# Performance work log

Hardware: AMD Instinct MI355X
Metric: run time of the kernel (lower is better)

Reference implementation:

```python
import jax, jax.numpy as jnp
import numpy as np

N = 50000      # nodes
E = 800000     # edges (avg degree 16)
IN, HID, OUT = 128, 128, 64


def setup_inputs() -> dict:
    key = jax.random.key(0)
    ks = jax.random.split(key, 6)
    x = jax.random.normal(ks[0], (N, IN), dtype=jnp.float32)
    edge_index = jax.random.randint(ks[1], (2, E), 0, N, dtype=jnp.int32)
    # GCNConv params (glorot-ish scaling)
    W1 = jax.random.normal(ks[2], (IN, HID), dtype=jnp.float32) * (1.0 / np.sqrt(IN))
    b1 = jnp.zeros((HID,), dtype=jnp.float32)
    W2 = jax.random.normal(ks[3], (HID, OUT), dtype=jnp.float32) * (1.0 / np.sqrt(HID))
    b2 = jnp.zeros((OUT,), dtype=jnp.float32)
    return {"x": x, "edge_index": edge_index, "W1": W1, "b1": b1, "W2": W2, "b2": b2}


def _gcn_conv(h, edge_index, W, b):
    """PyG GCNConv: linear transform, then sym-normalized aggregation with self-loops."""
    h = h @ W  # [N, out]
    src, dst = edge_index[0], edge_index[1]
    # degree including the added self-loop
    deg = jax.ops.segment_sum(jnp.ones((E,), h.dtype), dst, num_segments=N) + 1.0
    dinv = jax.lax.rsqrt(deg)                       # deg^{-1/2}
    norm = dinv[src] * dinv[dst]                    # [E]
    agg = jax.ops.segment_sum(h[src] * norm[:, None], dst, num_segments=N)
    agg = agg + h * (dinv * dinv)[:, None]          # self-loop term: deg^{-1} * h_i
    return agg + b


def reference(x, edge_index, W1, b1, W2, b2):
    h = jax.nn.relu(_gcn_conv(x, edge_index, W1, b1))
    h = jax.nn.relu(_gcn_conv(h, edge_index, W2, b2))
    return h
```

## Files before the change

kernel.cpp:

```cpp
#include <hip/hip_runtime.h>

#define DIN 128
#define DHID 128
#define DOUT 64
#define CAPB 6144
#define CHUNK 4096
#define EPT (CHUNK / 256)

typedef short bf16x8 __attribute__((ext_vector_type(8)));
typedef float f32x4 __attribute__((ext_vector_type(4)));

static __device__ __forceinline__ unsigned short f2bf(float f) {
  union { float f; unsigned u; } v; v.f = f;
  unsigned r = v.u + 0x7fffu + ((v.u >> 16) & 1u);
  return (unsigned short)(r >> 16);
}
static __device__ __forceinline__ float bf_lo(unsigned v) {
  union { unsigned u; float f; } t; t.u = v << 16; return t.f;
}
static __device__ __forceinline__ float bf_hi(unsigned v) {
  union { unsigned u; float f; } t; t.u = v & 0xffff0000u; return t.f;
}
static __device__ __forceinline__ float bf1(unsigned short v) {
  union { unsigned u; float f; } t; t.u = ((unsigned)v) << 16; return t.f;
}

static __device__ __forceinline__ void wcast_body(
    const float* __restrict__ W, unsigned short* __restrict__ Wf,
    int NOUT, int tid) {
  int f = tid >> 6;
  int lane = tid & 63;
  int t = f & 3;
  int nt = f >> 2;
  int kbase = t * 32 + (lane >> 4) * 8;
  int n = nt * 16 + (lane & 15);
#pragma unroll
  for (int j = 0; j < 8; ++j)
    Wf[(size_t)tid * 8 + j] = f2bf(W[(size_t)(kbase + j) * NOUT + n]);
}

__global__ __launch_bounds__(256) void init_kernel(
    const float* __restrict__ W1, const float* __restrict__ W2,
    unsigned short* __restrict__ Wf1, unsigned short* __restrict__ Wf2,
    int* __restrict__ bincursor) {
  const int b = blockIdx.x;
  const int t = threadIdx.x;
  if (b == 0) {
    bincursor[t] = 0;
  } else if (b <= 8) {
    wcast_body(W1, Wf1, DHID, (b - 1) * 256 + t);
  } else {
    wcast_body(W2, Wf2, DOUT, (b - 9) * 256 + t);
  }
}

static __device__ void gemm1_tile(
    const float* __restrict__ A, const unsigned short* __restrict__ Wf,
    unsigned short* __restrict__ C, int M, int tile) {
  constexpr int NT = DHID / 16;
  const int lane = threadIdx.x & 63;
  const int wave = threadIdx.x >> 6;
  const int g = lane >> 4;
  const int m15 = lane & 15;

  bf16x8 bfrag[NT * 4];
#pragma unroll
  for (int f = 0; f < NT * 4; ++f)
    bfrag[f] = *(const bf16x8*)(Wf + ((size_t)(f * 64 + lane)) * 8);

  const int rowbase = tile * 64 + wave * 16;
  if (rowbase >= M) return;
  f32x4 acc[NT];
#pragma unroll
  for (int nt = 0; nt < NT; ++nt) acc[nt] = (f32x4){0.f, 0.f, 0.f, 0.f};
  const float* arow = A + (size_t)(rowbase + m15) * 128 + g * 8;
  bf16x8 af[4];
#pragma unroll
  for (int t = 0; t < 4; ++t) {
    float4 a0 = *(const float4*)(arow + t * 32);
    float4 a1 = *(const float4*)(arow + t * 32 + 4);
    bf16x8 f;
    f[0] = (short)f2bf(a0.x); f[1] = (short)f2bf(a0.y);
    f[2] = (short)f2bf(a0.z); f[3] = (short)f2bf(a0.w);
    f[4] = (short)f2bf(a1.x); f[5] = (short)f2bf(a1.y);
    f[6] = (short)f2bf(a1.z); f[7] = (short)f2bf(a1.w);
    af[t] = f;
  }
#pragma unroll
  for (int t = 0; t < 4; ++t)
#pragma unroll
    for (int nt = 0; nt < NT; ++nt)
      acc[nt] = __builtin_amdgcn_mfma_f32_16x16x32_bf16(
          af[t], bfrag[nt * 4 + t], acc[nt], 0, 0, 0);
#pragma unroll
  for (int nt = 0; nt < NT; ++nt)
#pragma unroll
    for (int r = 0; r < 4; ++r) {
      int row = rowbase + g * 4 + r;
      if (row < M)
        C[(size_t)row * DHID + nt * 16 + m15] = f2bf(acc[nt][r]);
    }
}

__global__ __launch_bounds__(256) void phaseA_kernel(
    const int* __restrict__ src, const int* __restrict__ dst,
    int* __restrict__ bincursor, unsigned* __restrict__ binbuf, int E,
    int nbinA, const float* __restrict__ x,
    const unsigned short* __restrict__ Wf1, unsigned short* __restrict__ h1,
    int M) {
  __shared__ int hist[256];
  __shared__ int cnt[256];
  __shared__ int offs[256];
  __shared__ int cur[256];
  __shared__ int gbase[256];
  __shared__ unsigned stage[CHUNK];

  if ((int)blockIdx.x >= nbinA) {
    gemm1_tile(x, Wf1, h1, M, (int)blockIdx.x - nbinA);
    return;
  }

  const int t = threadIdx.x;
  const int base = blockIdx.x * CHUNK;
  const int n = min(CHUNK, E - base);

  hist[t] = 0;
  __syncthreads();

  unsigned rec[EPT];
  int rng[EPT];
#pragma unroll
  for (int j = 0; j < EPT; ++j) {
    int e = base + j * 256 + t;
    rng[j] = -1;
    if (e < E) {
      int d = dst[e];
      int s = src[e];
      int r = d >> 8;
      rng[j] = r;
      rec[j] = (unsigned)s | ((unsigned)(d & 255) << 16) | ((unsigned)r << 24);
      atomicAdd(&hist[r], 1);
    }
  }
  __syncthreads();
  int myc = hist[t];
  cnt[t] = myc;
  __syncthreads();
#pragma unroll
  for (int o = 1; o < 256; o <<= 1) {
    int u = (t >= o) ? hist[t - o] : 0;
    __syncthreads();
    hist[t] += u;
    __syncthreads();
  }
  offs[t] = hist[t] - myc;
  cur[t] = hist[t] - myc;
  __syncthreads();
#pragma unroll
  for (int j = 0; j < EPT; ++j) {
    if (rng[j] >= 0) {
      int pos = atomicAdd(&cur[rng[j]], 1);
      stage[pos] = rec[j];
    }
  }
  __syncthreads();
  int c = cnt[t];
  gbase[t] = c ? atomicAdd(&bincursor[t], c) : 0;
  __syncthreads();
  for (int i = t; i < n; i += 256) {
    unsigned v = stage[i];
    int r = v >> 24;
    int local = i - offs[r];
    int gpos = gbase[r] + local;
    if (gpos < CAPB) binbuf[(size_t)r * CAPB + gpos] = v & 0x00ffffffu;
  }
}

__global__ __launch_bounds__(256) void scan_local_kernel(
    const unsigned* __restrict__ binbuf, const int* __restrict__ bincursor,
    int* __restrict__ rowptr, int* __restrict__ bsum,
    float* __restrict__ dinv, int n) {
  __shared__ int deg[256];
  __shared__ int lds[256];
  const int t = threadIdx.x;
  const int b = blockIdx.x;
  deg[t] = 0;
  __syncthreads();
  const int cnt = min(bincursor[b], CAPB);
  const unsigned* seg = binbuf + (size_t)b * CAPB;
  for (int i = t; i < cnt; i += 256) atomicAdd(&deg[(seg[i] >> 16) & 0xff], 1);
  __syncthreads();
  const int i = b * 256 + t;
  int v = (i < n) ? deg[t] : 0;
  if (i < n) dinv[i] = rsqrtf((float)v + 1.0f);
  lds[t] = v;
  __syncthreads();
#pragma unroll
  for (int o = 1; o < 256; o <<= 1) {
    int u = (t >= o) ? lds[t - o] : 0;
    __syncthreads();
    lds[t] += u;
    __syncthreads();
  }
  if (i < n) rowptr[i] = lds[t] - v;
  if (t == 255) bsum[b] = lds[255];
}

__global__ __launch_bounds__(256) void scan_add_kernel(
    int* __restrict__ rowptr, const int* __restrict__ bsum, int nr,
    int n, int E) {
  __shared__ int lds[256];
  const int t = threadIdx.x;
  int v = (t < nr) ? bsum[t] : 0;
  lds[t] = v;
  __syncthreads();
#pragma unroll
  for (int o = 1; o < 256; o <<= 1) {
    int u = (t >= o) ? lds[t - o] : 0;
    __syncthreads();
    lds[t] += u;
    __syncthreads();
  }
  const int off = (blockIdx.x == 0) ? 0 : lds[blockIdx.x - 1];
  const int i = blockIdx.x * 256 + t;
  if (i < n) rowptr[i] += off;
  if (i == n) rowptr[n] = E;
}

__global__ __launch_bounds__(256) void binB_kernel(
    const unsigned* __restrict__ binbuf, const int* __restrict__ bincursor,
    const int* __restrict__ rowptr, const float* __restrict__ dinv,
    unsigned* __restrict__ recs, int n) {
  __shared__ int curs[256];
  __shared__ unsigned stage[CAPB];
  const int t = threadIdx.x;
  const int r = blockIdx.x;
  const int n0 = r * 256;
  const int nn = min(256, n - n0);
  const int segbase = rowptr[n0];
  if (t < nn) curs[t] = rowptr[n0 + t] - segbase;
  __syncthreads();
  const int cnt = min(bincursor[r], CAPB);
  const unsigned* seg = binbuf + (size_t)r * CAPB;
  for (int i = t; i < cnt; i += 256) {
    unsigned v = seg[i];
    int s = v & 0xffffu;
    int dl = (v >> 16) & 0xff;
    float w = dinv[s] * dinv[n0 + dl];
    int pos = atomicAdd(&curs[dl], 1);
    stage[pos] = (unsigned)s | ((unsigned)f2bf(w) << 16);
  }
  __syncthreads();
  for (int i = t; i < cnt; i += 256) recs[segbase + i] = stage[i];
}

__global__ __launch_bounds__(256) void agg1_gemm2_kernel(
    const unsigned short* __restrict__ h, const unsigned* __restrict__ recs,
    const int* __restrict__ rowptr, const float* __restrict__ dinv,
    const float* __restrict__ b1, const unsigned short* __restrict__ Wf2,
    unsigned short* __restrict__ h2, int n) {
  __shared__ unsigned short tile[16][136];
  const int wave = threadIdx.x >> 6;
  const int lane = threadIdx.x & 63;
  const int nbase = blockIdx.x * 16;
  const unsigned col = lane * 2;
  const float2 bv = *(const float2*)(b1 + col);

  for (int q = 0; q < 4; ++q) {
    const int row = wave * 4 + q;
    const int nid = nbase + row;
    if (nid >= n) break;
    const float di = dinv[nid];
    int p = rowptr[nid];
    const int end = rowptr[nid + 1];
    float ax = 0.f, ay = 0.f;
    for (; p < end && (p & 3); ++p) {
      unsigned r = recs[p];
      float w = bf_hi(r);
      unsigned v = *(const unsigned*)(h + (size_t)(r & 0xffffu) * 128 + col);
      ax += bf_lo(v) * w;
      ay += bf_hi(v) * w;
    }
    for (; p + 8 <= end; p += 8) {
      uint4 q0 = *(const uint4*)(recs + p);
      uint4 q1 = *(const uint4*)(recs + p + 4);
      unsigned v0 = *(const unsigned*)(h + (size_t)(q0.x & 0xffffu) * 128 + col);
      unsigned v1 = *(const unsigned*)(h + (size_t)(q0.y & 0xffffu) * 128 + col);
      unsigned v2 = *(const unsigned*)(h + (size_t)(q0.z & 0xffffu) * 128 + col);
      unsigned v3 = *(const unsigned*)(h + (size_t)(q0.w & 0xffffu) * 128 + col);
      unsigned v4 = *(const unsigned*)(h + (size_t)(q1.x & 0xffffu) * 128 + col);
      unsigned v5 = *(const unsigned*)(h + (size_t)(q1.y & 0xffffu) * 128 + col);
      unsigned v6 = *(const unsigned*)(h + (size_t)(q1.z & 0xffffu) * 128 + col);
      unsigned v7 = *(const unsigned*)(h + (size_t)(q1.w & 0xffffu) * 128 + col);
      ax += bf_lo(v0) * bf_hi(q0.x) + bf_lo(v1) * bf_hi(q0.y) +
            bf_lo(v2) * bf_hi(q0.z) + bf_lo(v3) * bf_hi(q0.w);
      ay += bf_hi(v0) * bf_hi(q0.x) + bf_hi(v1) * bf_hi(q0.y) +
            bf_hi(v2) * bf_hi(q0.z) + bf_hi(v3) * bf_hi(q0.w);
      ax += bf_lo(v4) * bf_hi(q1.x) + bf_lo(v5) * bf_hi(q1.y) +
            bf_lo(v6) * bf_hi(q1.z) + bf_lo(v7) * bf_hi(q1.w);
      ay += bf_hi(v4) * bf_hi(q1.x) + bf_hi(v5) * bf_hi(q1.y) +
            bf_hi(v6) * bf_hi(q1.z) + bf_hi(v7) * bf_hi(q1.w);
    }
    for (; p + 4 <= end; p += 4) {
      uint4 q0 = *(const uint4*)(recs + p);
      unsigned v0 = *(const unsigned*)(h + (size_t)(q0.x & 0xffffu) * 128 + col);
      unsigned v1 = *(const unsigned*)(h + (size_t)(q0.y & 0xffffu) * 128 + col);
      unsigned v2 = *(const unsigned*)(h + (size_t)(q0.z & 0xffffu) * 128 + col);
      unsigned v3 = *(const unsigned*)(h + (size_t)(q0.w & 0xffffu) * 128 + col);
      ax += bf_lo(v0) * bf_hi(q0.x) + bf_lo(v1) * bf_hi(q0.y) +
            bf_lo(v2) * bf_hi(q0.z) + bf_lo(v3) * bf_hi(q0.w);
      ay += bf_hi(v0) * bf_hi(q0.x) + bf_hi(v1) * bf_hi(q0.y) +
            bf_hi(v2) * bf_hi(q0.z) + bf_hi(v3) * bf_hi(q0.w);
    }
    for (; p < end; ++p) {
      unsigned r = recs[p];
      float w = bf_hi(r);
      unsigned v = *(const unsigned*)(h + (size_t)(r & 0xffffu) * 128 + col);
      ax += bf_lo(v) * w;
      ay += bf_hi(v) * w;
    }
    float w2 = di * di;
    unsigned v = *(const unsigned*)(h + (size_t)nid * 128 + col);
    ax += bf_lo(v) * w2;
    ay += bf_hi(v) * w2;
    ax = fmaxf(ax + bv.x, 0.f);
    ay = fmaxf(ay + bv.y, 0.f);
    unsigned pk = ((unsigned)f2bf(ay) << 16) | f2bf(ax);
    *(unsigned*)&tile[row][col] = pk;
  }
  __syncthreads();

  const int g = lane >> 4;
  const int m15 = lane & 15;
  f32x4 acc = (f32x4){0.f, 0.f, 0.f, 0.f};
#pragma unroll
  for (int t = 0; t < 4; ++t) {
    bf16x8 af = *(const bf16x8*)&tile[m15][t * 32 + g * 8];
    bf16x8 bf = *(const bf16x8*)(Wf2 + ((size_t)((wave * 4 + t) * 64 + lane)) * 8);
    acc = __builtin_amdgcn_mfma_f32_16x16x32_bf16(af, bf, acc, 0, 0, 0);
  }
#pragma unroll
  for (int r = 0; r < 4; ++r) {
    int row = nbase + g * 4 + r;
    if (row < n) h2[(size_t)row * DOUT + wave * 16 + m15] = f2bf(acc[r]);
  }
}

__global__ __launch_bounds__(256) void aggregate2_kernel(
    const unsigned short* __restrict__ h, const unsigned* __restrict__ recs,
    const int* __restrict__ rowptr, const float* __restrict__ dinv,
    const float* __restrict__ bias, float* __restrict__ out, int n) {
  const int wave = threadIdx.x >> 6;
  const int lane = threadIdx.x & 63;
  const int nid = blockIdx.x * 4 + wave;
  if (nid >= n) return;

  const float di = dinv[nid];
  int p = rowptr[nid];
  const int end = rowptr[nid + 1];

  float acc = 0.f;
  for (; p < end && (p & 3); ++p) {
    unsigned r = recs[p];
    acc += bf1(h[(size_t)(r & 0xffffu) * 64 + lane]) * bf_hi(r);
  }
  for (; p + 8 <= end; p += 8) {
    uint4 q0 = *(const uint4*)(recs + p);
    uint4 q1 = *(const uint4*)(recs + p + 4);
    unsigned short v0 = h[(size_t)(q0.x & 0xffffu) * 64 + lane];
    unsigned short v1 = h[(size_t)(q0.y & 0xffffu) * 64 + lane];
    unsigned short v2 = h[(size_t)(q0.z & 0xffffu) * 64 + lane];
    unsigned short v3 = h[(size_t)(q0.w & 0xffffu) * 64 + lane];
    unsigned short v4 = h[(size_t)(q1.x & 0xffffu) * 64 + lane];
    unsigned short v5 = h[(size_t)(q1.y & 0xffffu) * 64 + lane];
    unsigned short v6 = h[(size_t)(q1.z & 0xffffu) * 64 + lane];
    unsigned short v7 = h[(size_t)(q1.w & 0xffffu) * 64 + lane];
    acc += bf1(v0) * bf_hi(q0.x) + bf1(v1) * bf_hi(q0.y) +
           bf1(v2) * bf_hi(q0.z) + bf1(v3) * bf_hi(q0.w);
    acc += bf1(v4) * bf_hi(q1.x) + bf1(v5) * bf_hi(q1.y) +
           bf1(v6) * bf_hi(q1.z) + bf1(v7) * bf_hi(q1.w);
  }
  for (; p + 4 <= end; p += 4) {
    uint4 q0 = *(const uint4*)(recs + p);
    unsigned short v0 = h[(size_t)(q0.x & 0xffffu) * 64 + lane];
    unsigned short v1 = h[(size_t)(q0.y & 0xffffu) * 64 + lane];
    unsigned short v2 = h[(size_t)(q0.z & 0xffffu) * 64 + lane];
    unsigned short v3 = h[(size_t)(q0.w & 0xffffu) * 64 + lane];
    acc += bf1(v0) * bf_hi(q0.x) + bf1(v1) * bf_hi(q0.y) +
           bf1(v2) * bf_hi(q0.z) + bf1(v3) * bf_hi(q0.w);
  }
  for (; p < end; ++p) {
    unsigned r = recs[p];
    acc += bf1(h[(size_t)(r & 0xffffu) * 64 + lane]) * bf_hi(r);
  }
  acc += bf1(h[(size_t)nid * 64 + lane]) * di * di;
  acc = fmaxf(acc + bias[lane], 0.f);
  out[(size_t)nid * 64 + lane] = acc;
}

extern "C" void kernel_launch(void* const* d_in, const int* in_sizes, int n_in,
                              void* d_out, int out_size, void* d_ws, size_t ws_size,
                              hipStream_t stream) {
  const float* x = (const float*)d_in[0];
  const int* edge = (const int*)d_in[1];
  const float* W1 = (const float*)d_in[2];
  const float* b1 = (const float*)d_in[3];
  const float* W2 = (const float*)d_in[4];
  const float* b2 = (const float*)d_in[5];
  float* out = (float*)d_out;

  const int N = in_sizes[0] / DIN;
  const int E = in_sizes[1] / 2;
  const int* src = edge;
  const int* dst = edge + E;
  const int NR = (N + 255) >> 8;
  const int nbinA = (E + CHUNK - 1) / CHUNK;
  const int ntiles1 = (N + 63) / 64;

  char* base = (char*)d_ws;
  size_t off = 0;
  auto carve = [&](size_t bytes) {
    char* p = base + off;
    off += (bytes + 255) & ~(size_t)255;
    return p;
  };
  float* dinv = (float*)carve((size_t)N * 4);
  int* rowptr = (int*)carve((size_t)(N + 1) * 4);
  int* bsum = (int*)carve(256 * 4);
  int* bincursor = (int*)carve(256 * 4);
  unsigned* binbuf = (unsigned*)carve((size_t)NR * CAPB * 4 + CAPB * 4);
  unsigned* recs = (unsigned*)carve((size_t)E * 4);
  unsigned short* h1 = (unsigned short*)carve((size_t)N * DHID * 2);
  unsigned short* h2 = (unsigned short*)carve((size_t)N * DOUT * 2);
  unsigned short* Wf1 = (unsigned short*)carve((size_t)DIN * DHID * 2);
  unsigned short* Wf2 = (unsigned short*)carve((size_t)DHID * DOUT * 2);

  init_kernel<<<13, 256, 0, stream>>>(W1, W2, Wf1, Wf2, bincursor);
  phaseA_kernel<<<nbinA + ntiles1, 256, 0, stream>>>(
      src, dst, bincursor, binbuf, E, nbinA, x, Wf1, h1, N);
  scan_local_kernel<<<NR, 256, 0, stream>>>(binbuf, bincursor, rowptr, bsum, dinv, N);
  scan_add_kernel<<<(N + 256) / 256, 256, 0, stream>>>(rowptr, bsum, NR, N, E);
  binB_kernel<<<NR, 256, 0, stream>>>(binbuf, bincursor, rowptr, dinv, recs, N);
  agg1_gemm2_kernel<<<(N + 15) / 16, 256, 0, stream>>>(
      h1, recs, rowptr, dinv, b1, Wf2, h2, N);
  aggregate2_kernel<<<(N + 3) / 4, 256, 0, stream>>>(
      h2, recs, rowptr, dinv, b2, out, N);
}
```

Baseline: 189.4 us.

## Fold block-offset scan into binB kernel and unroll gather loops to 16

Removes the separate scan_add kernel launch by having each binB block redundantly scan the per-bin block sums and apply its own offset to rowptr while building local cursors. It also widens the main edge-gather loops in both aggregation kernels from 8 to 16 records per iteration and hoists the column/lane offset into a base pointer, to keep more independent loads in flight. The change saves one launch and one pass over rowptr at the cost of a small redundant scan per block and higher register pressure in the aggregation loops.

```diff
diff --git a/kernel.cpp b/kernel.cpp
--- a/kernel.cpp
+++ b/kernel.cpp
@@ -206,39 +206,37 @@
   if (t == 255) bsum[b] = lds[255];
 }
 
-__global__ __launch_bounds__(256) void scan_add_kernel(
-    int* __restrict__ rowptr, const int* __restrict__ bsum, int nr,
-    int n, int E) {
-  __shared__ int lds[256];
-  const int t = threadIdx.x;
-  int v = (t < nr) ? bsum[t] : 0;
-  lds[t] = v;
-  __syncthreads();
-#pragma unroll
-  for (int o = 1; o < 256; o <<= 1) {
-    int u = (t >= o) ? lds[t - o] : 0;
-    __syncthreads();
-    lds[t] += u;
-    __syncthreads();
-  }
-  const int off = (blockIdx.x == 0) ? 0 : lds[blockIdx.x - 1];
-  const int i = blockIdx.x * 256 + t;
-  if (i < n) rowptr[i] += off;
-  if (i == n) rowptr[n] = E;
-}
-
 __global__ __launch_bounds__(256) void binB_kernel(
     const unsigned* __restrict__ binbuf, const int* __restrict__ bincursor,
-    const int* __restrict__ rowptr, const float* __restrict__ dinv,
-    unsigned* __restrict__ recs, int n) {
+    int* __restrict__ rowptr, const int* __restrict__ bsum, int nr,
+    const float* __restrict__ dinv, unsigned* __restrict__ recs, int n) {
   __shared__ int curs[256];
+  __shared__ int bscan[256];
   __shared__ unsigned stage[CAPB];
   const int t = threadIdx.x;
   const int r = blockIdx.x;
   const int n0 = r * 256;
   const int nn = min(256, n - n0);
-  const int segbase = rowptr[n0];
-  if (t < nn) curs[t] = rowptr[n0 + t] - segbase;
+
+  int bv = (t < nr) ? bsum[t] : 0;
+  bscan[t] = bv;
+  __syncthreads();
+#pragma unroll
+  for (int o = 1; o < 256; o <<= 1) {
+    int u = (t >= o) ? bscan[t - o] : 0;
+    __syncthreads();
+    bscan[t] += u;
+    __syncthreads();
+  }
+  const int segbase = (r == 0) ? 0 : bscan[r - 1];
+
+  int local = 0;
+  if (t < nn) {
+    local = rowptr[n0 + t];
+    curs[t] = local;
+    rowptr[n0 + t] = local + segbase;
+  }
+  if (r == nr - 1 && t == 0) rowptr[n] = bscan[nr - 1];
   __syncthreads();
   const int cnt = min(bincursor[r], CAPB);
   const unsigned* seg = binbuf + (size_t)r * CAPB;
@@ -265,6 +263,7 @@
   const int nbase = blockIdx.x * 16;
   const unsigned col = lane * 2;
   const float2 bv = *(const float2*)(b1 + col);
+  const unsigned short* hc = h + col;
 
   for (int q = 0; q < 4; ++q) {
     const int row = wave * 4 + q;
@@ -277,21 +276,31 @@
     for (; p < end && (p & 3); ++p) {
       unsigned r = recs[p];
       float w = bf_hi(r);
-      unsigned v = *(const unsigned*)(h + (size_t)(r & 0xffffu) * 128 + col);
+      unsigned v = *(const unsigned*)(hc + (size_t)(r & 0xffffu) * 128);
       ax += bf_lo(v) * w;
       ay += bf_hi(v) * w;
     }
-    for (; p + 8 <= end; p += 8) {
+    for (; p + 16 <= end; p += 16) {
       uint4 q0 = *(const uint4*)(recs + p);
       uint4 q1 = *(const uint4*)(recs + p + 4);
-      unsigned v0 = *(const unsigned*)(h + (size_t)(q0.x & 0xffffu) * 128 + col);
-      unsigned v1 = *(const unsigned*)(h + (size_t)(q0.y & 0xffffu) * 128 + col);
-      unsigned v2 = *(const unsigned*)(h + (size_t)(q0.z & 0xffffu) * 128 + col);
-      unsigned v3 = *(const unsigned*)(h + (size_t)(q0.w & 0xffffu) * 128 + col);
-      unsigned v4 = *(const unsigned*)(h + (size_t)(q1.x & 0xffffu) * 128 + col);
-      unsigned v5 = *(const unsigned*)(h + (size_t)(q1.y & 0xffffu) * 128 + col);
-      unsigned v6 = *(const unsigned*)(h + (size_t)(q1.z & 0xffffu) * 128 + col);
-      unsigned v7 = *(const unsigned*)(h + (size_t)(q1.w & 0xffffu) * 128 + col);
+      uint4 q2 = *(const uint4*)(recs + p + 8);
+      uint4 q3 = *(const uint4*)(recs + p + 12);
+      unsigned v0 = *(const unsigned*)(hc + (size_t)(q0.x & 0xffffu) * 128);
+      unsigned v1 = *(const unsigned*)(hc + (size_t)(q0.y & 0xffffu) * 128);
+      unsigned v2 = *(const unsigned*)(hc + (size_t)(q0.z & 0xffffu) * 128);
+      unsigned v3 = *(const unsigned*)(hc + (size_t)(q0.w & 0xffffu) * 128);
+      unsigned v4 = *(const unsigned*)(hc + (size_t)(q1.x & 0xffffu) * 128);
+      unsigned v5 = *(const unsigned*)(hc + (size_t)(q1.y & 0xffffu) * 128);
+      unsigned v6 = *(const unsigned*)(hc + (size_t)(q1.z & 0xffffu) * 128);
+      unsigned v7 = *(const unsigned*)(hc + (size_t)(q1.w & 0xffffu) * 128);
+      unsigned v8 = *(const unsigned*)(hc + (size_t)(q2.x & 0xffffu) * 128);
+      unsigned v9 = *(const unsigned*)(hc + (size_t)(q2.y & 0xffffu) * 128);
+      unsigned va = *(const unsigned*)(hc + (size_t)(q2.z & 0xffffu) * 128);
+      unsigned vb = *(const unsigned*)(hc + (size_t)(q2.w & 0xffffu) * 128);
+      unsigned vc = *(const unsigned*)(hc + (size_t)(q3.x & 0xffffu) * 128);
+      unsigned vd = *(const unsigned*)(hc + (size_t)(q3.y & 0xffffu) * 128);
+      unsigned ve = *(const unsigned*)(hc + (size_t)(q3.z & 0xffffu) * 128);
+      unsigned vf = *(const unsigned*)(hc + (size_t)(q3.w & 0xffffu) * 128);
       ax += bf_lo(v0) * bf_hi(q0.x) + bf_lo(v1) * bf_hi(q0.y) +
             bf_lo(v2) * bf_hi(q0.z) + bf_lo(v3) * bf_hi(q0.w);
       ay += bf_hi(v0) * bf_hi(q0.x) + bf_hi(v1) * bf_hi(q0.y) +
@@ -300,13 +309,21 @@
             bf_lo(v6) * bf_hi(q1.z) + bf_lo(v7) * bf_hi(q1.w);
       ay += bf_hi(v4) * bf_hi(q1.x) + bf_hi(v5) * bf_hi(q1.y) +
             bf_hi(v6) * bf_hi(q1.z) + bf_hi(v7) * bf_hi(q1.w);
+      ax += bf_lo(v8) * bf_hi(q2.x) + bf_lo(v9) * bf_hi(q2.y) +
+            bf_lo(va) * bf_hi(q2.z) + bf_lo(vb) * bf_hi(q2.w);
+      ay += bf_hi(v8) * bf_hi(q2.x) + bf_hi(v9) * bf_hi(q2.y) +
+            bf_hi(va) * bf_hi(q2.z) + bf_hi(vb) * bf_hi(q2.w);
+      ax += bf_lo(vc) * bf_hi(q3.x) + bf_lo(vd) * bf_hi(q3.y) +
+            bf_lo(ve) * bf_hi(q3.z) + bf_lo(vf) * bf_hi(q3.w);
+      ay += bf_hi(vc) * bf_hi(q3.x) + bf_hi(vd) * bf_hi(q3.y) +
+            bf_hi(ve) * bf_hi(q3.z) + bf_hi(vf) * bf_hi(q3.w);
     }
     for (; p + 4 <= end; p += 4) {
       uint4 q0 = *(const uint4*)(recs + p);
-      unsigned v0 = *(const unsigned*)(h + (size_t)(q0.x & 0xffffu) * 128 + col);
-      unsigned v1 = *(const unsigned*)(h + (size_t)(q0.y & 0xffffu) * 128 + col);
-      unsigned v2 = *(const unsigned*)(h + (size_t)(q0.z & 0xffffu) * 128 + col);
-      unsigned v3 = *(const unsigned*)(h + (size_t)(q0.w & 0xffffu) * 128 + col);
+      unsigned v0 = *(const unsigned*)(hc + (size_t)(q0.x & 0xffffu) * 128);
+      unsigned v1 = *(const unsigned*)(hc + (size_t)(q0.y & 0xffffu) * 128);
+      unsigned v2 = *(const unsigned*)(hc + (size_t)(q0.z & 0xffffu) * 128);
+      unsigned v3 = *(const unsigned*)(hc + (size_t)(q0.w & 0xffffu) * 128);
       ax += bf_lo(v0) * bf_hi(q0.x) + bf_lo(v1) * bf_hi(q0.y) +
             bf_lo(v2) * bf_hi(q0.z) + bf_lo(v3) * bf_hi(q0.w);
       ay += bf_hi(v0) * bf_hi(q0.x) + bf_hi(v1) * bf_hi(q0.y) +
@@ -315,12 +332,12 @@
     for (; p < end; ++p) {
       unsigned r = recs[p];
       float w = bf_hi(r);
-      unsigned v = *(const unsigned*)(h + (size_t)(r & 0xffffu) * 128 + col);
+      unsigned v = *(const unsigned*)(hc + (size_t)(r & 0xffffu) * 128);
       ax += bf_lo(v) * w;
       ay += bf_hi(v) * w;
     }
     float w2 = di * di;
-    unsigned v = *(const unsigned*)(h + (size_t)nid * 128 + col);
+    unsigned v = *(const unsigned*)(hc + (size_t)nid * 128);
     ax += bf_lo(v) * w2;
     ay += bf_hi(v) * w2;
     ax = fmaxf(ax + bv.x, 0.f);
@@ -358,42 +375,57 @@
   const float di = dinv[nid];
   int p = rowptr[nid];
   const int end = rowptr[nid + 1];
+  const unsigned short* hl = h + lane;
 
   float acc = 0.f;
   for (; p < end && (p & 3); ++p) {
     unsigned r = recs[p];
-    acc += bf1(h[(size_t)(r & 0xffffu) * 64 + lane]) * bf_hi(r);
-  }
-  for (; p + 8 <= end; p += 8) {
+    acc += bf1(hl[(size_t)(r & 0xffffu) * 64]) * bf_hi(r);
+  }
+  for (; p + 16 <= end; p += 16) {
     uint4 q0 = *(const uint4*)(recs + p);
     uint4 q1 = *(const uint4*)(recs + p + 4);
-    unsigned short v0 = h[(size_t)(q0.x & 0xffffu) * 64 + lane];
-    unsigned short v1 = h[(size_t)(q0.y & 0xffffu) * 64 + lane];
-    unsigned short v2 = h[(size_t)(q0.z & 0xffffu) * 64 + lane];
-    unsigned short v3 = h[(size_t)(q0.w & 0xffffu) * 64 + lane];
-    unsigned short v4 = h[(size_t)(q1.x & 0xffffu) * 64 + lane];
-    unsigned short v5 = h[(size_t)(q1.y & 0xffffu) * 64 + lane];
-    unsigned short v6 = h[(size_t)(q1.z & 0xffffu) * 64 + lane];
-    unsigned short v7 = h[(size_t)(q1.w & 0xffffu) * 64 + lane];
+    uint4 q2 = *(const uint4*)(recs + p + 8);
+    uint4 q3 = *(const uint4*)(recs + p + 12);
+    unsigned short v0 = hl[(size_t)(q0.x & 0xffffu) * 64];
+    unsigned short v1 = hl[(size_t)(q0.y & 0xffffu) * 64];
+    unsigned short v2 = hl[(size_t)(q0.z & 0xffffu) * 64];
+    unsigned short v3 = hl[(size_t)(q0.w & 0xffffu) * 64];
+    unsigned short v4 = hl[(size_t)(q1.x & 0xffffu) * 64];
+    unsigned short v5 = hl[(size_t)(q1.y & 0xffffu) * 64];
+    unsigned short v6 = hl[(size_t)(q1.z & 0xffffu) * 64];
+    unsigned short v7 = hl[(size_t)(q1.w & 0xffffu) * 64];
+    unsigned short v8 = hl[(size_t)(q2.x & 0xffffu) * 64];
+    unsigned short v9 = hl[(size_t)(q2.y & 0xffffu) * 64];
+    unsigned short va = hl[(size_t)(q2.z & 0xffffu) * 64];
+    unsigned short vb = hl[(size_t)(q2.w & 0xffffu) * 64];
+    unsigned short vc = hl[(size_t)(q3.x & 0xffffu) * 64];
+    unsigned short vd = hl[(size_t)(q3.y & 0xffffu) * 64];
+    unsigned short ve = hl[(size_t)(q3.z & 0xffffu) * 64];
+    unsigned short vf = hl[(size_t)(q3.w & 0xffffu) * 64];
     acc += bf1(v0) * bf_hi(q0.x) + bf1(v1) * bf_hi(q0.y) +
            bf1(v2) * bf_hi(q0.z) + bf1(v3) * bf_hi(q0.w);
     acc += bf1(v4) * bf_hi(q1.x) + bf1(v5) * bf_hi(q1.y) +
            bf1(v6) * bf_hi(q1.z) + bf1(v7) * bf_hi(q1.w);
+    acc += bf1(v8) * bf_hi(q2.x) + bf1(v9) * bf_hi(q2.y) +
+           bf1(va) * bf_hi(q2.z) + bf1(vb) * bf_hi(q2.w);
+    acc += bf1(vc) * bf_hi(q3.x) + bf1(vd) * bf_hi(q3.y) +
+           bf1(ve) * bf_hi(q3.z) + bf1(vf) * bf_hi(q3.w);
   }
   for (; p + 4 <= end; p += 4) {
     uint4 q0 = *(const uint4*)(recs + p);
-    unsigned short v0 = h[(size_t)(q0.x & 0xffffu) * 64 + lane];
-    unsigned short v1 = h[(size_t)(q0.y & 0xffffu) * 64 + lane];
-    unsigned short v2 = h[(size_t)(q0.z & 0xffffu) * 64 + lane];
-    unsigned short v3 = h[(size_t)(q0.w & 0xffffu) * 64 + lane];
+    unsigned short v0 = hl[(size_t)(q0.x & 0xffffu) * 64];
+    unsigned short v1 = hl[(size_t)(q0.y & 0xffffu) * 64];
+    unsigned short v2 = hl[(size_t)(q0.z & 0xffffu) * 64];
+    unsigned short v3 = hl[(size_t)(q0.w & 0xffffu) * 64];
     acc += bf1(v0) * bf_hi(q0.x) + bf1(v1) * bf_hi(q0.y) +
            bf1(v2) * bf_hi(q0.z) + bf1(v3) * bf_hi(q0.w);
   }
   for (; p < end; ++p) {
     unsigned r = recs[p];
-    acc += bf1(h[(size_t)(r & 0xffffu) * 64 + lane]) * bf_hi(r);
-  }
-  acc += bf1(h[(size_t)nid * 64 + lane]) * di * di;
+    acc += bf1(hl[(size_t)(r & 0xffffu) * 64]) * bf_hi(r);
+  }
+  acc += bf1(hl[(size_t)nid * 64]) * di * di;
   acc = fmaxf(acc + bias[lane], 0.f);
   out[(size_t)nid * 64 + lane] = acc;
 }
@@ -439,8 +471,7 @@
   phaseA_kernel<<<nbinA + ntiles1, 256, 0, stream>>>(
       src, dst, bincursor, binbuf, E, nbinA, x, Wf1, h1, N);
   scan_local_kernel<<<NR, 256, 0, stream>>>(binbuf, bincursor, rowptr, bsum, dinv, N);
-  scan_add_kernel<<<(N + 256) / 256, 256, 0, stream>>>(rowptr, bsum, NR, N, E);
-  binB_kernel<<<NR, 256, 0, stream>>>(binbuf, bincursor, rowptr, dinv, recs, N);
+  binB_kernel<<<NR, 256, 0, stream>>>(binbuf, bincursor, rowptr, bsum, NR, dinv, recs, N);
   agg1_gemm2_kernel<<<(N + 15) / 16, 256, 0, stream>>>(
       h1, recs, rowptr, dinv, b1, Wf2, h2, N);
   aggregate2_kernel<<<(N + 3) / 4, 256, 0, stream>>>(
```

New measurement: 190.5 us. Within noise of the previous version (+0.6%).

## Split each wave across two edge halves in aggregation and fuse scan-add into binB

Applied to the files above, without the earlier changes.

The two aggregation kernels now split each wave into two half-waves that process alternate groups of 8 edges. Each lane loads wider per-lane feature slices (8 bytes for layer 1, 4 bytes for layer 2), and the halves are combined with a cross-lane shuffle. Edge tails are masked with clamped indices and zero weights instead of separate alignment and remainder loops. The separate scan_add kernel is removed: binB re-scans the block sums, fixes rowptr and writes the final entry itself, saving one launch. The risk is wasted masked loads on low-degree nodes and half the lanes sitting idle during the epilogue.

```diff
diff --git a/kernel.cpp b/kernel.cpp
--- a/kernel.cpp
+++ b/kernel.cpp
@@ -20,9 +20,6 @@
 }
 static __device__ __forceinline__ float bf_hi(unsigned v) {
   union { unsigned u; float f; } t; t.u = v & 0xffff0000u; return t.f;
-}
-static __device__ __forceinline__ float bf1(unsigned short v) {
-  union { unsigned u; float f; } t; t.u = ((unsigned)v) << 16; return t.f;
 }
 
 static __device__ __forceinline__ void wcast_body(
@@ -206,39 +203,36 @@
   if (t == 255) bsum[b] = lds[255];
 }
 
-__global__ __launch_bounds__(256) void scan_add_kernel(
-    int* __restrict__ rowptr, const int* __restrict__ bsum, int nr,
-    int n, int E) {
-  __shared__ int lds[256];
-  const int t = threadIdx.x;
-  int v = (t < nr) ? bsum[t] : 0;
-  lds[t] = v;
-  __syncthreads();
-#pragma unroll
-  for (int o = 1; o < 256; o <<= 1) {
-    int u = (t >= o) ? lds[t - o] : 0;
-    __syncthreads();
-    lds[t] += u;
-    __syncthreads();
-  }
-  const int off = (blockIdx.x == 0) ? 0 : lds[blockIdx.x - 1];
-  const int i = blockIdx.x * 256 + t;
-  if (i < n) rowptr[i] += off;
-  if (i == n) rowptr[n] = E;
-}
-
 __global__ __launch_bounds__(256) void binB_kernel(
     const unsigned* __restrict__ binbuf, const int* __restrict__ bincursor,
-    const int* __restrict__ rowptr, const float* __restrict__ dinv,
-    unsigned* __restrict__ recs, int n) {
+    int* __restrict__ rowptr, const int* __restrict__ bsum, int nr,
+    const float* __restrict__ dinv, unsigned* __restrict__ recs, int n) {
   __shared__ int curs[256];
+  __shared__ int bscan[256];
   __shared__ unsigned stage[CAPB];
   const int t = threadIdx.x;
   const int r = blockIdx.x;
   const int n0 = r * 256;
   const int nn = min(256, n - n0);
-  const int segbase = rowptr[n0];
-  if (t < nn) curs[t] = rowptr[n0 + t] - segbase;
+
+  int bv = (t < nr) ? bsum[t] : 0;
+  bscan[t] = bv;
+  __syncthreads();
+#pragma unroll
+  for (int o = 1; o < 256; o <<= 1) {
+    int u = (t >= o) ? bscan[t - o] : 0;
+    __syncthreads();
+    bscan[t] += u;
+    __syncthreads();
+  }
+  const int segbase = (r == 0) ? 0 : bscan[r - 1];
+
+  if (t < nn) {
+    int local = rowptr[n0 + t];
+    curs[t] = local;
+    rowptr[n0 + t] = local + segbase;
+  }
+  if (r == nr - 1 && t == 0) rowptr[n] = bscan[nr - 1];
   __syncthreads();
   const int cnt = min(bincursor[r], CAPB);
   const unsigned* seg = binbuf + (size_t)r * CAPB;
@@ -262,71 +256,61 @@
   __shared__ unsigned short tile[16][136];
   const int wave = threadIdx.x >> 6;
   const int lane = threadIdx.x & 63;
+  const int sub = lane >> 5;
+  const int c = lane & 31;
   const int nbase = blockIdx.x * 16;
-  const unsigned col = lane * 2;
-  const float2 bv = *(const float2*)(b1 + col);
+  const unsigned short* hc = h + c * 4;
 
   for (int q = 0; q < 4; ++q) {
     const int row = wave * 4 + q;
     const int nid = nbase + row;
     if (nid >= n) break;
     const float di = dinv[nid];
-    int p = rowptr[nid];
+    const int p0 = rowptr[nid];
     const int end = rowptr[nid + 1];
-    float ax = 0.f, ay = 0.f;
-    for (; p < end && (p & 3); ++p) {
-      unsigned r = recs[p];
-      float w = bf_hi(r);
-      unsigned v = *(const unsigned*)(h + (size_t)(r & 0xffffu) * 128 + col);
-      ax += bf_lo(v) * w;
-      ay += bf_hi(v) * w;
-    }
-    for (; p + 8 <= end; p += 8) {
-      uint4 q0 = *(const uint4*)(recs + p);
-      uint4 q1 = *(const uint4*)(recs + p + 4);
-      unsigned v0 = *(const unsigned*)(h + (size_t)(q0.x & 0xffffu) * 128 + col);
-      unsigned v1 = *(const unsigned*)(h + (size_t)(q0.y & 0xffffu) * 128 + col);
-      unsigned v2 = *(const unsigned*)(h + (size_t)(q0.z & 0xffffu) * 128 + col);
-      unsigned v3 = *(const unsigned*)(h + (size_t)(q0.w & 0xffffu) * 128 + col);
-      unsigned v4 = *(const unsigned*)(h + (size_t)(q1.x & 0xffffu) * 128 + col);
-      unsigned v5 = *(const unsigned*)(h + (size_t)(q1.y & 0xffffu) * 128 + col);
-      unsigned v6 = *(const unsigned*)(h + (size_t)(q1.z & 0xffffu) * 128 + col);
-      unsigned v7 = *(const unsigned*)(h + (size_t)(q1.w & 0xffffu) * 128 + col);
-      ax += bf_lo(v0) * bf_hi(q0.x) + bf_lo(v1) * bf_hi(q0.y) +
-            bf_lo(v2) * bf_hi(q0.z) + bf_lo(v3) * bf_hi(q0.w);
-      ay += bf_hi(v0) * bf_hi(q0.x) + bf_hi(v1) * bf_hi(q0.y) +
-            bf_hi(v2) * bf_hi(q0.z) + bf_hi(v3) * bf_hi(q0.w);
-      ax += bf_lo(v4) * bf_hi(q1.x) + bf_lo(v5) * bf_hi(q1.y) +
-            bf_lo(v6) * bf_hi(q1.z) + bf_lo(v7) * bf_hi(q1.w);
-      ay += bf_hi(v4) * bf_hi(q1.x) + bf_hi(v5) * bf_hi(q1.y) +
-            bf_hi(v6) * bf_hi(q1.z) + bf_hi(v7) * bf_hi(q1.w);
-    }
-    for (; p + 4 <= end; p += 4) {
-      uint4 q0 = *(const uint4*)(recs + p);
-      unsigned v0 = *(const unsigned*)(h + (size_t)(q0.x & 0xffffu) * 128 + col);
-      unsigned v1 = *(const unsigned*)(h + (size_t)(q0.y & 0xffffu) * 128 + col);
-      unsigned v2 = *(const unsigned*)(h + (size_t)(q0.z & 0xffffu) * 128 + col);
-      unsigned v3 = *(const unsigned*)(h + (size_t)(q0.w & 0xffffu) * 128 + col);
-      ax += bf_lo(v0) * bf_hi(q0.x) + bf_lo(v1) * bf_hi(q0.y) +
-            bf_lo(v2) * bf_hi(q0.z) + bf_lo(v3) * bf_hi(q0.w);
-      ay += bf_hi(v0) * bf_hi(q0.x) + bf_hi(v1) * bf_hi(q0.y) +
-            bf_hi(v2) * bf_hi(q0.z) + bf_hi(v3) * bf_hi(q0.w);
-    }
-    for (; p < end; ++p) {
-      unsigned r = recs[p];
-      float w = bf_hi(r);
-      unsigned v = *(const unsigned*)(h + (size_t)(r & 0xffffu) * 128 + col);
-      ax += bf_lo(v) * w;
-      ay += bf_hi(v) * w;
-    }
-    float w2 = di * di;
-    unsigned v = *(const unsigned*)(h + (size_t)nid * 128 + col);
-    ax += bf_lo(v) * w2;
-    ay += bf_hi(v) * w2;
-    ax = fmaxf(ax + bv.x, 0.f);
-    ay = fmaxf(ay + bv.y, 0.f);
-    unsigned pk = ((unsigned)f2bf(ay) << 16) | f2bf(ax);
-    *(unsigned*)&tile[row][col] = pk;
+    const int d = end - p0;
+    float a0 = 0.f, a1 = 0.f, a2 = 0.f, a3 = 0.f;
+    const int nb = (d + 15) >> 4;
+    for (int b = 0; b < nb; ++b) {
+      const int pb = p0 + (b << 4) + (sub << 3);
+#pragma unroll
+      for (int j = 0; j < 8; ++j) {
+        int ei = pb + j;
+        int ec = min(ei, end - 1);
+        unsigned r = recs[ec];
+        float w = (ei < end) ? bf_hi(r) : 0.f;
+        const unsigned* vp = (const unsigned*)(hc + (size_t)(r & 0xffffu) * 128);
+        unsigned u0 = vp[0];
+        unsigned u1 = vp[1];
+        a0 += bf_lo(u0) * w;
+        a1 += bf_hi(u0) * w;
+        a2 += bf_lo(u1) * w;
+        a3 += bf_hi(u1) * w;
+      }
+    }
+    a0 += __shfl_xor(a0, 32, 64);
+    a1 += __shfl_xor(a1, 32, 64);
+    a2 += __shfl_xor(a2, 32, 64);
+    a3 += __shfl_xor(a3, 32, 64);
+    if (sub == 0) {
+      const unsigned* vp = (const unsigned*)(hc + (size_t)nid * 128);
+      unsigned u0 = vp[0];
+      unsigned u1 = vp[1];
+      float w2 = di * di;
+      a0 += bf_lo(u0) * w2;
+      a1 += bf_hi(u0) * w2;
+      a2 += bf_lo(u1) * w2;
+      a3 += bf_hi(u1) * w2;
+      float4 bv = *(const float4*)(b1 + c * 4);
+      a0 = fmaxf(a0 + bv.x, 0.f);
+      a1 = fmaxf(a1 + bv.y, 0.f);
+      a2 = fmaxf(a2 + bv.z, 0.f);
+      a3 = fmaxf(a3 + bv.w, 0.f);
+      uint2 pk;
+      pk.x = ((unsigned)f2bf(a1) << 16) | f2bf(a0);
+      pk.y = ((unsigned)f2bf(a3) << 16) | f2bf(a2);
+      *(uint2*)&tile[row][c * 4] = pk;
+    }
   }
   __syncthreads();
 
@@ -352,50 +336,44 @@
     const float* __restrict__ bias, float* __restrict__ out, int n) {
   const int wave = threadIdx.x >> 6;
   const int lane = threadIdx.x & 63;
+  const int sub = lane >> 5;
+  const int c = lane & 31;
   const int nid = blockIdx.x * 4 + wave;
   if (nid >= n) return;
 
   const float di = dinv[nid];
-  int p = rowptr[nid];
+  const int p0 = rowptr[nid];
   const int end = rowptr[nid + 1];
-
-  float acc = 0.f;
-  for (; p < end && (p & 3); ++p) {
-    unsigned r = recs[p];
-    acc += bf1(h[(size_t)(r & 0xffffu) * 64 + lane]) * bf_hi(r);
-  }
-  for (; p + 8 <= end; p += 8) {
-    uint4 q0 = *(const uint4*)(recs + p);
-    uint4 q1 = *(const uint4*)(recs + p + 4);
-    unsigned short v0 = h[(size_t)(q0.x & 0xffffu) * 64 + lane];
-    unsigned short v1 = h[(size_t)(q0.y & 0xffffu) * 64 + lane];
-    unsigned short v2 = h[(size_t)(q0.z & 0xffffu) * 64 + lane];
-    unsigned short v3 = h[(size_t)(q0.w & 0xffffu) * 64 + lane];
-    unsigned short v4 = h[(size_t)(q1.x & 0xffffu) * 64 + lane];
-    unsigned short v5 = h[(size_t)(q1.y & 0xffffu) * 64 + lane];
-    unsigned short v6 = h[(size_t)(q1.z & 0xffffu) * 64 + lane];
-    unsigned short v7 = h[(size_t)(q1.w & 0xffffu) * 64 + lane];
-    acc += bf1(v0) * bf_hi(q0.x) + bf1(v1) * bf_hi(q0.y) +
-           bf1(v2) * bf_hi(q0.z) + bf1(v3) * bf_hi(q0.w);
-    acc += bf1(v4) * bf_hi(q1.x) + bf1(v5) * bf_hi(q1.y) +
-           bf1(v6) * bf_hi(q1.z) + bf1(v7) * bf_hi(q1.w);
-  }
-  for (; p + 4 <= end; p += 4) {
-    uint4 q0 = *(const uint4*)(recs + p);
-    unsigned short v0 = h[(size_t)(q0.x & 0xffffu) * 64 + lane];
-    unsigned short v1 = h[(size_t)(q0.y & 0xffffu) * 64 + lane];
-    unsigned short v2 = h[(size_t)(q0.z & 0xffffu) * 64 + lane];
-    unsigned short v3 = h[(size_t)(q0.w & 0xffffu) * 64 + lane];
-    acc += bf1(v0) * bf_hi(q0.x) + bf1(v1) * bf_hi(q0.y) +
-           bf1(v2) * bf_hi(q0.z) + bf1(v3) * bf_hi(q0.w);
-  }
-  for (; p < end; ++p) {
-    unsigned r = recs[p];
-    acc += bf1(h[(size_t)(r & 0xffffu) * 64 + lane]) * bf_hi(r);
-  }
-  acc += bf1(h[(size_t)nid * 64 + lane]) * di * di;
-  acc = fmaxf(acc + bias[lane], 0.f);
-  out[(size_t)nid * 64 + lane] = acc;
+  const int d = end - p0;
+  const unsigned short* hc = h + c * 2;
+
+  float a0 = 0.f, a1 = 0.f;
+  const int nb = (d + 15) >> 4;
+  for (int b = 0; b < nb; ++b) {
+    const int pb = p0 + (b << 4) + (sub << 3);
+#pragma unroll
+    for (int j = 0; j < 8; ++j) {
+      int ei = pb + j;
+      int ec = min(ei, end - 1);
+      unsigned r = recs[ec];
+      float w = (ei < end) ? bf_hi(r) : 0.f;
+      unsigned v = *(const unsigned*)(hc + (size_t)(r & 0xffffu) * 64);
+      a0 += bf_lo(v) * w;
+      a1 += bf_hi(v) * w;
+    }
+  }
+  a0 += __shfl_xor(a0, 32, 64);
+  a1 += __shfl_xor(a1, 32, 64);
+  if (sub == 0) {
+    unsigned v = *(const unsigned*)(hc + (size_t)nid * 64);
+    float w2 = di * di;
+    a0 += bf_lo(v) * w2;
+    a1 += bf_hi(v) * w2;
+    float2 bv = *(const float2*)(bias + c * 2);
+    a0 = fmaxf(a0 + bv.x, 0.f);
+    a1 = fmaxf(a1 + bv.y, 0.f);
+    *(float2*)(out + (size_t)nid * 64 + c * 2) = make_float2(a0, a1);
+  }
 }
 
 extern "C" void kernel_launch(void* const* d_in, const int* in_sizes, int n_in,
@@ -439,8 +417,7 @@
   phaseA_kernel<<<nbinA + ntiles1, 256, 0, stream>>>(
       src, dst, bincursor, binbuf, E, nbinA, x, Wf1, h1, N);
   scan_local_kernel<<<NR, 256, 0, stream>>>(binbuf, bincursor, rowptr, bsum, dinv, N);
-  scan_add_kernel<<<(N + 256) / 256, 256, 0, stream>>>(rowptr, bsum, NR, N, E);
-  binB_kernel<<<NR, 256, 0, stream>>>(binbuf, bincursor, rowptr, dinv, recs, N);
+  binB_kernel<<<NR, 256, 0, stream>>>(binbuf, bincursor, rowptr, bsum, NR, dinv, recs, N);
   agg1_gemm2_kernel<<<(N + 15) / 16, 256, 0, stream>>>(
       h1, recs, rowptr, dinv, b1, Wf2, h2, N);
   aggregate2_kernel<<<(N + 3) / 4, 256, 0, stream>>>(
```

Result: faster. 168.8 us (-10.9%).
